# Optimization experiments

Hardware: AMD Instinct MI355X
Metric: run time of the kernel (lower is better)

Reference implementation:

```python
import jax, jax.numpy as jnp
import numpy as np

H = 768
L = 4096
P, KP = 8192, 8
EV, KE = 2048, 6
E = 16384
NR = 32
NUM_LABELS = 2


def setup_inputs() -> dict:
    key = jax.random.key(0)
    ks = jax.random.split(key, 10)
    seq = jax.random.normal(ks[0], (1, L, H), dtype=jnp.float32)
    phrase_idx = jax.random.randint(ks[1], (P, KP), 0, L, dtype=jnp.int32)
    phrase_mask = jnp.ones((P, KP), dtype=jnp.float32)
    event_idx = jax.random.randint(ks[2], (EV, KE), 0, L, dtype=jnp.int32)
    event_mask = jnp.ones((EV, KE), dtype=jnp.float32)
    pair_idx = jax.random.randint(ks[3], (E, 2), 0, EV, dtype=jnp.int32)
    root_idx = jax.random.randint(ks[4], (NR,), 0, P, dtype=jnp.int32)
    s1 = 1.0 / np.sqrt(2 * H)
    W1 = jax.random.normal(ks[5], (2 * H, H), dtype=jnp.float32) * s1
    b1 = jnp.zeros((H,), dtype=jnp.float32)
    Wb = jax.random.normal(ks[6], (2 * H, NUM_LABELS), dtype=jnp.float32) * s1
    bb = jnp.zeros((NUM_LABELS,), dtype=jnp.float32)
    return {"seq": seq, "phrase_idx": phrase_idx, "phrase_mask": phrase_mask,
            "event_idx": event_idx, "event_mask": event_mask, "pair_idx": pair_idx,
            "root_idx": root_idx, "W1": W1, "b1": b1, "Wb": Wb, "bb": bb}


def _masked_mean_gather(tok, idx, mask):
    # tok: [L,H]; idx: [N,K] int; mask: [N,K] float -> [N,H]
    g = tok[idx]                                  # [N,K,H] irregular gather
    s = jnp.einsum('nkh,nk->nh', g, mask)
    d = jnp.maximum(mask.sum(axis=1, keepdims=True), 1.0)
    return s / d


def reference(seq, phrase_idx, phrase_mask, event_idx, event_mask, pair_idx,
              root_idx, W1, b1, Wb, bb):
    tok = seq[0]                                   # [L,H] doc token embeddings
    # phrase embeddings: gather token indices per phrase, masked mean-pool
    ph = _masked_mean_gather(tok, phrase_idx, phrase_mask)   # [P,H]
    # event embeddings: gather span tokens per event, masked mean-pool
    ev = _masked_mean_gather(tok, event_idx, event_mask)     # [EV,H]
    # event-pair nodes: concat the two event embeddings, middle_layer MLP
    e1 = ev[pair_idx[:, 0]]                        # [E,H]
    e2 = ev[pair_idx[:, 1]]                        # [E,H]
    pairs = jnp.concatenate([e1, e2], axis=-1)     # [E,2H]
    node = jax.nn.relu(pairs @ W1 + b1)            # [E,H] (dropout inactive at eval)
    # virtual root: mean of sentence-root phrase embeddings
    vroot = ph[root_idx].mean(axis=0)              # [H]
    feat = jnp.concatenate([node, jnp.broadcast_to(vroot, node.shape)], axis=-1)
    logits = feat @ Wb + bb                        # [E,NUM_LABELS] bilinear classifier
    return logits
```

## Files before the change

### kernel.cpp

```cpp
#include <hip/hip_runtime.h>
#include <hip/hip_bf16.h>

#define H   768
#define H4  192
#define EVN 2048
#define KE  6
#define KP  8
#define EE  16384
#define NR  32

typedef __bf16 v8bf __attribute__((ext_vector_type(8)));
typedef float  v4f  __attribute__((ext_vector_type(4)));

__device__ __forceinline__ void gload16(const void* g, void* lds) {
    __builtin_amdgcn_global_load_lds(
        (const __attribute__((address_space(1))) void*)g,
        (__attribute__((address_space(3))) void*)lds, 16, 0, 0);
}
__device__ __forceinline__ float blo(unsigned u) {
    return __uint_as_float(u << 16);
}
__device__ __forceinline__ float bhi(unsigned u) {
    return __uint_as_float(u & 0xffff0000u);
}

__global__ __launch_bounds__(256) void pre_kernel(
    const float* __restrict__ seq,
    const int* __restrict__ eidx, const float* __restrict__ emask,
    const int* __restrict__ pidx, const float* __restrict__ pmask,
    const int* __restrict__ root_idx, const float* __restrict__ W1,
    __hip_bfloat16* __restrict__ evb, __hip_bfloat16* __restrict__ Wt,
    float* __restrict__ phr) {
    __shared__ float tile[64][65];
    const int b = blockIdx.x;
    const int t = threadIdx.x;
    const float4* seq4 = (const float4*)seq;

    if (b < 512) {
        const int w = t >> 6, l = t & 63;
        const int n = b * 4 + w;
        int idx[KE]; float mk[KE]; float ms = 0.f;
#pragma unroll
        for (int k = 0; k < KE; ++k) {
            idx[k] = eidx[n * KE + k];
            mk[k]  = emask[n * KE + k];
            ms    += mk[k];
        }
        const float inv = 1.f / fmaxf(ms, 1.f);
#pragma unroll
        for (int g = 0; g < 3; ++g) {
            const int t4 = l + g * 64;
            float4 acc = {0.f, 0.f, 0.f, 0.f};
#pragma unroll
            for (int k = 0; k < KE; ++k) {
                float4 v = seq4[idx[k] * H4 + t4];
                acc.x = fmaf(mk[k], v.x, acc.x);
                acc.y = fmaf(mk[k], v.y, acc.y);
                acc.z = fmaf(mk[k], v.z, acc.z);
                acc.w = fmaf(mk[k], v.w, acc.w);
            }
            __hip_bfloat16 o[4];
            o[0] = __float2bfloat16(acc.x * inv);
            o[1] = __float2bfloat16(acc.y * inv);
            o[2] = __float2bfloat16(acc.z * inv);
            o[3] = __float2bfloat16(acc.w * inv);
            *(uint2*)&evb[n * H + t4 * 4] = *(uint2*)o;
        }
    } else if (b < 520) {
        const int w = t >> 6, l = t & 63;
        const int r = (b - 512) * 4 + w;
        const int pr = root_idx[r];
        int idx[KP]; float mk[KP]; float ms = 0.f;
#pragma unroll
        for (int k = 0; k < KP; ++k) {
            idx[k] = pidx[pr * KP + k];
            mk[k]  = pmask[pr * KP + k];
            ms    += mk[k];
        }
        const float inv = 1.f / fmaxf(ms, 1.f);
#pragma unroll
        for (int g = 0; g < 3; ++g) {
            const int t4 = l + g * 64;
            float4 acc = {0.f, 0.f, 0.f, 0.f};
#pragma unroll
            for (int k = 0; k < KP; ++k) {
                float4 v = seq4[idx[k] * H4 + t4];
                acc.x = fmaf(mk[k], v.x, acc.x);
                acc.y = fmaf(mk[k], v.y, acc.y);
                acc.z = fmaf(mk[k], v.z, acc.z);
                acc.w = fmaf(mk[k], v.w, acc.w);
            }
            float4 o = {acc.x * inv, acc.y * inv, acc.z * inv, acc.w * inv};
            ((float4*)phr)[r * H4 + t4] = o;
        }
    } else {
        const int b2 = b - 520;
        const int k0 = (b2 % 12) * 64;
        const int j0 = (b2 / 12) * 64;
        const int s  = (j0 >= H) ? H : 0;
        const int n0 = j0 - s;
        const int c  = t & 63;
        const int r0 = t >> 6;
#pragma unroll
        for (int i = 0; i < 16; ++i) {
            const int r = r0 + i * 4;
            tile[r][c] = W1[(size_t)(s + k0 + r) * H + n0 + c];
        }
        __syncthreads();
#pragma unroll
        for (int i = 0; i < 16; ++i) {
            const int r = r0 + i * 4;
            Wt[(size_t)(j0 + r) * H + k0 + c] = __float2bfloat16(tile[c][r]);
        }
    }
}

__global__ __launch_bounds__(256) void gemm_kernel(
    const __hip_bfloat16* __restrict__ evb_,
    const __hip_bfloat16* __restrict__ Wt_,
    const float* __restrict__ b1v,
    const float* __restrict__ phr, const float* __restrict__ Wb,
    const float* __restrict__ bbv,
    __hip_bfloat16* __restrict__ evw, float* __restrict__ cvec) {
    if (blockIdx.x == 384) {
        __shared__ float r0s[256], r1s[256];
        const int t = threadIdx.x;
        float p0 = 0.f, p1 = 0.f;
#pragma unroll
        for (int w = 0; w < 3; ++w) {
            const int d = t + w * 256;
            float s = 0.f;
            for (int r = 0; r < NR; ++r) s += phr[r * H + d];
            const float v = s * (1.0f / NR);
            p0 = fmaf(v, Wb[(H + d) * 2 + 0], p0);
            p1 = fmaf(v, Wb[(H + d) * 2 + 1], p1);
        }
        r0s[t] = p0; r1s[t] = p1;
        __syncthreads();
        for (int off = 128; off > 0; off >>= 1) {
            if (t < off) { r0s[t] += r0s[t + off]; r1s[t] += r1s[t + off]; }
            __syncthreads();
        }
        if (t == 0) { cvec[0] = r0s[0] + bbv[0]; cvec[1] = r1s[0] + bbv[1]; }
        return;
    }

    __shared__ short As[2][8192];
    __shared__ short Bs[2][4096];
    const short* evb = (const short*)evb_;
    const short* Wt  = (const short*)Wt_;

    const int bid = blockIdx.x;
    const int swz = (bid & 7) * 48 + (bid >> 3);
    const int mt = swz / 24, nt = swz % 24;
    const int m0 = mt * 128, n0 = nt * 64;

    const int t = threadIdx.x;
    const int l = t & 63;
    const int w = t >> 6;
    const int wr = (w >> 1) * 64;
    const int wc = (w & 1) * 32;

    const short* aSrc[4]; int aOff[4];
    const short* bSrc[2]; int bOff[2];
#pragma unroll
    for (int c = 0; c < 4; ++c) {
        const int s = c * 256 + t;
        const int r = s >> 3, pg = s & 7, g = pg ^ (r & 7);
        aSrc[c] = evb + (size_t)(m0 + r) * H + g * 8;
        aOff[c] = s * 16;
    }
#pragma unroll
    for (int c = 0; c < 2; ++c) {
        const int s = c * 256 + t;
        const int r = s >> 3, pg = s & 7, g = pg ^ (r & 7);
        bSrc[c] = Wt + (size_t)(n0 + r) * H + g * 8;
        bOff[c] = s * 16;
    }

    const int fr = l & 15, gq = l >> 4, xm = fr & 7;
    int aRow[4], bRow[2];
#pragma unroll
    for (int mi = 0; mi < 4; ++mi) aRow[mi] = (wr + mi * 16 + fr) * 64;
#pragma unroll
    for (int nj = 0; nj < 2; ++nj) bRow[nj] = (wc + nj * 16 + fr) * 64;
    const int pga = (gq ^ xm) * 8;
    const int pgb = ((4 + gq) ^ xm) * 8;

    v4f acc[4][2] = {};

#pragma unroll
    for (int c = 0; c < 4; ++c) gload16(aSrc[c], (char*)As[0] + aOff[c]);
#pragma unroll
    for (int c = 0; c < 2; ++c) gload16(bSrc[c], (char*)Bs[0] + bOff[c]);
    __syncthreads();

    for (int ks = 0; ks < 12; ++ks) {
        const int cur = ks & 1;
        if (ks < 11) {
#pragma unroll
            for (int c = 0; c < 4; ++c)
                gload16(aSrc[c] + (ks + 1) * 64, (char*)As[cur ^ 1] + aOff[c]);
#pragma unroll
            for (int c = 0; c < 2; ++c)
                gload16(bSrc[c] + (ks + 1) * 64, (char*)Bs[cur ^ 1] + bOff[c]);
        }
        const short* Ab = As[cur];
        const short* Bb = Bs[cur];
        {
            v8bf a0 = *(const v8bf*)(Ab + aRow[0] + pga);
            v8bf a1 = *(const v8bf*)(Ab + aRow[1] + pga);
            v8bf a2 = *(const v8bf*)(Ab + aRow[2] + pga);
            v8bf a3 = *(const v8bf*)(Ab + aRow[3] + pga);
            v8bf b0 = *(const v8bf*)(Bb + bRow[0] + pga);
            v8bf b1 = *(const v8bf*)(Bb + bRow[1] + pga);
            acc[0][0] = __builtin_amdgcn_mfma_f32_16x16x32_bf16(a0, b0, acc[0][0], 0, 0, 0);
            acc[0][1] = __builtin_amdgcn_mfma_f32_16x16x32_bf16(a0, b1, acc[0][1], 0, 0, 0);
            acc[1][0] = __builtin_amdgcn_mfma_f32_16x16x32_bf16(a1, b0, acc[1][0], 0, 0, 0);
            acc[1][1] = __builtin_amdgcn_mfma_f32_16x16x32_bf16(a1, b1, acc[1][1], 0, 0, 0);
            acc[2][0] = __builtin_amdgcn_mfma_f32_16x16x32_bf16(a2, b0, acc[2][0], 0, 0, 0);
            acc[2][1] = __builtin_amdgcn_mfma_f32_16x16x32_bf16(a2, b1, acc[2][1], 0, 0, 0);
            acc[3][0] = __builtin_amdgcn_mfma_f32_16x16x32_bf16(a3, b0, acc[3][0], 0, 0, 0);
            acc[3][1] = __builtin_amdgcn_mfma_f32_16x16x32_bf16(a3, b1, acc[3][1], 0, 0, 0);
        }
        {
            v8bf a0 = *(const v8bf*)(Ab + aRow[0] + pgb);
            v8bf a1 = *(const v8bf*)(Ab + aRow[1] + pgb);
            v8bf a2 = *(const v8bf*)(Ab + aRow[2] + pgb);
            v8bf a3 = *(const v8bf*)(Ab + aRow[3] + pgb);
            v8bf b0 = *(const v8bf*)(Bb + bRow[0] + pgb);
            v8bf b1 = *(const v8bf*)(Bb + bRow[1] + pgb);
            acc[0][0] = __builtin_amdgcn_mfma_f32_16x16x32_bf16(a0, b0, acc[0][0], 0, 0, 0);
            acc[0][1] = __builtin_amdgcn_mfma_f32_16x16x32_bf16(a0, b1, acc[0][1], 0, 0, 0);
            acc[1][0] = __builtin_amdgcn_mfma_f32_16x16x32_bf16(a1, b0, acc[1][0], 0, 0, 0);
            acc[1][1] = __builtin_amdgcn_mfma_f32_16x16x32_bf16(a1, b1, acc[1][1], 0, 0, 0);
            acc[2][0] = __builtin_amdgcn_mfma_f32_16x16x32_bf16(a2, b0, acc[2][0], 0, 0, 0);
            acc[2][1] = __builtin_amdgcn_mfma_f32_16x16x32_bf16(a2, b1, acc[2][1], 0, 0, 0);
            acc[3][0] = __builtin_amdgcn_mfma_f32_16x16x32_bf16(a3, b0, acc[3][0], 0, 0, 0);
            acc[3][1] = __builtin_amdgcn_mfma_f32_16x16x32_bf16(a3, b1, acc[3][1], 0, 0, 0);
        }
        __syncthreads();
    }

    float bv[2];
#pragma unroll
    for (int nj = 0; nj < 2; ++nj) {
        const int ocol = n0 + wc + nj * 16 + fr;
        bv[nj] = (ocol >= H) ? b1v[ocol - H] : 0.f;
    }
#pragma unroll
    for (int mi = 0; mi < 4; ++mi)
#pragma unroll
        for (int nj = 0; nj < 2; ++nj) {
            const int ocol = n0 + wc + nj * 16 + fr;
#pragma unroll
            for (int r = 0; r < 4; ++r) {
                const int orow = m0 + wr + mi * 16 + gq * 4 + r;
                evw[(size_t)orow * 1536 + ocol] =
                    __float2bfloat16(acc[mi][nj][r] + bv[nj]);
            }
        }
}

__global__ __launch_bounds__(256) void pair_logits_kernel(
    const __hip_bfloat16* __restrict__ evw_, const int* __restrict__ pair_idx,
    const float* __restrict__ Wb, const float* __restrict__ cvec,
    float* __restrict__ out) {
    const ushort* evw = (const ushort*)evw_;
    const int wave = threadIdx.x >> 6;
    const int lane = threadIdx.x & 63;
    const int i = blockIdx.x * 4 + wave;
    const int p0 = pair_idx[i * 2 + 0];
    const int p1 = pair_idx[i * 2 + 1];
    const ushort* ra = evw + (size_t)p0 * 1536;
    const ushort* rb = evw + (size_t)p1 * 1536 + H;
    float acc0 = 0.f, acc1 = 0.f;
#pragma unroll
    for (int h = 0; h < 2; ++h) {
        const int j = h * 384 + lane * 6;
        uint3 ua = *(const uint3*)(ra + j);
        uint3 ub = *(const uint3*)(rb + j);
        float4 w0 = *(const float4*)(Wb + j * 2);
        float4 w1 = *(const float4*)(Wb + j * 2 + 4);
        float4 w2 = *(const float4*)(Wb + j * 2 + 8);
        float n0 = fmaxf(blo(ua.x) + blo(ub.x), 0.f);
        float n1 = fmaxf(bhi(ua.x) + bhi(ub.x), 0.f);
        float n2 = fmaxf(blo(ua.y) + blo(ub.y), 0.f);
        float n3 = fmaxf(bhi(ua.y) + bhi(ub.y), 0.f);
        float n4 = fmaxf(blo(ua.z) + blo(ub.z), 0.f);
        float n5 = fmaxf(bhi(ua.z) + bhi(ub.z), 0.f);
        acc0 += n0 * w0.x + n1 * w0.z + n2 * w1.x + n3 * w1.z + n4 * w2.x + n5 * w2.z;
        acc1 += n0 * w0.y + n1 * w0.w + n2 * w1.y + n3 * w1.w + n4 * w2.y + n5 * w2.w;
    }
#pragma unroll
    for (int off = 32; off > 0; off >>= 1) {
        acc0 += __shfl_xor(acc0, off, 64);
        acc1 += __shfl_xor(acc1, off, 64);
    }
    if (lane == 0) {
        out[i * 2 + 0] = acc0 + cvec[0];
        out[i * 2 + 1] = acc1 + cvec[1];
    }
}

extern "C" void kernel_launch(void* const* d_in, const int* in_sizes, int n_in,
                              void* d_out, int out_size, void* d_ws, size_t ws_size,
                              hipStream_t stream) {
    const float* seq         = (const float*)d_in[0];
    const int*   phrase_idx  = (const int*)  d_in[1];
    const float* phrase_mask = (const float*)d_in[2];
    const int*   event_idx   = (const int*)  d_in[3];
    const float* event_mask  = (const float*)d_in[4];
    const int*   pair_idx    = (const int*)  d_in[5];
    const int*   root_idx    = (const int*)  d_in[6];
    const float* W1          = (const float*)d_in[7];
    const float* b1          = (const float*)d_in[8];
    const float* Wb          = (const float*)d_in[9];
    const float* bb          = (const float*)d_in[10];
    float* out = (float*)d_out;

    char* wsb = (char*)d_ws;
    __hip_bfloat16* evb = (__hip_bfloat16*)wsb;
    __hip_bfloat16* Wt  = (__hip_bfloat16*)(wsb + 3145728);
    __hip_bfloat16* evw = (__hip_bfloat16*)(wsb + 5505024);
    float* phr = (float*)(wsb + 11796480);
    float* c   = (float*)(wsb + 11894784);

    pre_kernel<<<808, 256, 0, stream>>>(seq, event_idx, event_mask,
                                        phrase_idx, phrase_mask, root_idx,
                                        W1, evb, Wt, phr);
    gemm_kernel<<<385, 256, 0, stream>>>(evb, Wt, b1, phr, Wb, bb, evw, c);
    pair_logits_kernel<<<EE / 4, 256, 0, stream>>>(evw, pair_idx, Wb, c, out);
}
```

Before: 34.39 us.

## Load B operand directly into registers and double K-step to 128

The GEMM no longer stages the weight (B) tile through LDS. Each lane loads its B fragments straight from global memory into double-buffered registers. The A tile K-step grows from 64 to 128 with a 16-way XOR swizzle, which halves the number of barriers and iterations, and the K loop is fully unrolled. This removes the LDS traffic and the LDS writes for B, but it raises VGPR pressure (16 v8bf B registers) and depends on uncoalesced per-lane global loads being hidden by the prefetch.

```diff
diff --git a/kernel.cpp b/kernel.cpp
--- a/kernel.cpp
+++ b/kernel.cpp
@@ -122,8 +122,11 @@
     const float* __restrict__ phr, const float* __restrict__ Wb,
     const float* __restrict__ bbv,
     __hip_bfloat16* __restrict__ evw, float* __restrict__ cvec) {
+    __shared__ short As[2][16384];
+
     if (blockIdx.x == 384) {
-        __shared__ float r0s[256], r1s[256];
+        float* r0s = (float*)&As[0][0];
+        float* r1s = r0s + 256;
         const int t = threadIdx.x;
         float p0 = 0.f, p1 = 0.f;
 #pragma unroll
@@ -145,8 +148,6 @@
         return;
     }
 
-    __shared__ short As[2][8192];
-    __shared__ short Bs[2][4096];
     const short* evb = (const short*)evb_;
     const short* Wt  = (const short*)Wt_;
 
@@ -161,75 +162,63 @@
     const int wr = (w >> 1) * 64;
     const int wc = (w & 1) * 32;
 
-    const short* aSrc[4]; int aOff[4];
-    const short* bSrc[2]; int bOff[2];
-#pragma unroll
-    for (int c = 0; c < 4; ++c) {
+    const short* aSrc[8]; int aOff[8];
+#pragma unroll
+    for (int c = 0; c < 8; ++c) {
         const int s = c * 256 + t;
-        const int r = s >> 3, pg = s & 7, g = pg ^ (r & 7);
+        const int r = s >> 4, pg = s & 15, g = pg ^ (r & 15);
         aSrc[c] = evb + (size_t)(m0 + r) * H + g * 8;
         aOff[c] = s * 16;
     }
-#pragma unroll
-    for (int c = 0; c < 2; ++c) {
-        const int s = c * 256 + t;
-        const int r = s >> 3, pg = s & 7, g = pg ^ (r & 7);
-        bSrc[c] = Wt + (size_t)(n0 + r) * H + g * 8;
-        bOff[c] = s * 16;
-    }
-
-    const int fr = l & 15, gq = l >> 4, xm = fr & 7;
-    int aRow[4], bRow[2];
-#pragma unroll
-    for (int mi = 0; mi < 4; ++mi) aRow[mi] = (wr + mi * 16 + fr) * 64;
-#pragma unroll
-    for (int nj = 0; nj < 2; ++nj) bRow[nj] = (wc + nj * 16 + fr) * 64;
-    const int pga = (gq ^ xm) * 8;
-    const int pgb = ((4 + gq) ^ xm) * 8;
+
+    const int fr = l & 15, gq = l >> 4, xm = fr & 15;
+    int aRowB[4];
+#pragma unroll
+    for (int mi = 0; mi < 4; ++mi) aRowB[mi] = (wr + mi * 16 + fr) * 256;
+
+    const short* bPtr[2];
+#pragma unroll
+    for (int nj = 0; nj < 2; ++nj)
+        bPtr[nj] = Wt + (size_t)(n0 + wc + nj * 16 + fr) * H + gq * 8;
 
     v4f acc[4][2] = {};
-
-#pragma unroll
-    for (int c = 0; c < 4; ++c) gload16(aSrc[c], (char*)As[0] + aOff[c]);
-#pragma unroll
-    for (int c = 0; c < 2; ++c) gload16(bSrc[c], (char*)Bs[0] + bOff[c]);
+    v8bf bEven[2][4], bOdd[2][4];
+
+#pragma unroll
+    for (int nj = 0; nj < 2; ++nj)
+#pragma unroll
+        for (int h = 0; h < 4; ++h)
+            bEven[nj][h] = *(const v8bf*)(bPtr[nj] + h * 32);
+
+#pragma unroll
+    for (int c = 0; c < 8; ++c) gload16(aSrc[c], (char*)As[0] + aOff[c]);
     __syncthreads();
 
-    for (int ks = 0; ks < 12; ++ks) {
+#pragma unroll
+    for (int ks = 0; ks < 6; ++ks) {
         const int cur = ks & 1;
-        if (ks < 11) {
-#pragma unroll
-            for (int c = 0; c < 4; ++c)
-                gload16(aSrc[c] + (ks + 1) * 64, (char*)As[cur ^ 1] + aOff[c]);
-#pragma unroll
-            for (int c = 0; c < 2; ++c)
-                gload16(bSrc[c] + (ks + 1) * 64, (char*)Bs[cur ^ 1] + bOff[c]);
-        }
-        const short* Ab = As[cur];
-        const short* Bb = Bs[cur];
-        {
-            v8bf a0 = *(const v8bf*)(Ab + aRow[0] + pga);
-            v8bf a1 = *(const v8bf*)(Ab + aRow[1] + pga);
-            v8bf a2 = *(const v8bf*)(Ab + aRow[2] + pga);
-            v8bf a3 = *(const v8bf*)(Ab + aRow[3] + pga);
-            v8bf b0 = *(const v8bf*)(Bb + bRow[0] + pga);
-            v8bf b1 = *(const v8bf*)(Bb + bRow[1] + pga);
-            acc[0][0] = __builtin_amdgcn_mfma_f32_16x16x32_bf16(a0, b0, acc[0][0], 0, 0, 0);
-            acc[0][1] = __builtin_amdgcn_mfma_f32_16x16x32_bf16(a0, b1, acc[0][1], 0, 0, 0);
-            acc[1][0] = __builtin_amdgcn_mfma_f32_16x16x32_bf16(a1, b0, acc[1][0], 0, 0, 0);
-            acc[1][1] = __builtin_amdgcn_mfma_f32_16x16x32_bf16(a1, b1, acc[1][1], 0, 0, 0);
-            acc[2][0] = __builtin_amdgcn_mfma_f32_16x16x32_bf16(a2, b0, acc[2][0], 0, 0, 0);
-            acc[2][1] = __builtin_amdgcn_mfma_f32_16x16x32_bf16(a2, b1, acc[2][1], 0, 0, 0);
-            acc[3][0] = __builtin_amdgcn_mfma_f32_16x16x32_bf16(a3, b0, acc[3][0], 0, 0, 0);
-            acc[3][1] = __builtin_amdgcn_mfma_f32_16x16x32_bf16(a3, b1, acc[3][1], 0, 0, 0);
-        }
-        {
-            v8bf a0 = *(const v8bf*)(Ab + aRow[0] + pgb);
-            v8bf a1 = *(const v8bf*)(Ab + aRow[1] + pgb);
-            v8bf a2 = *(const v8bf*)(Ab + aRow[2] + pgb);
-            v8bf a3 = *(const v8bf*)(Ab + aRow[3] + pgb);
-            v8bf b0 = *(const v8bf*)(Bb + bRow[0] + pgb);
-            v8bf b1 = *(const v8bf*)(Bb + bRow[1] + pgb);
+        if (ks < 5) {
+#pragma unroll
+            for (int c = 0; c < 8; ++c)
+                gload16(aSrc[c] + (ks + 1) * 128, (char*)As[cur ^ 1] + aOff[c]);
+#pragma unroll
+            for (int nj = 0; nj < 2; ++nj)
+#pragma unroll
+                for (int h = 0; h < 4; ++h) {
+                    v8bf v = *(const v8bf*)(bPtr[nj] + (ks + 1) * 128 + h * 32);
+                    if (cur) bEven[nj][h] = v; else bOdd[nj][h] = v;
+                }
+        }
+        const char* Ab = (const char*)As[cur];
+#pragma unroll
+        for (int h = 0; h < 4; ++h) {
+            const int pgo = ((h * 4 + gq) ^ xm) * 16;
+            v8bf a0 = *(const v8bf*)(Ab + aRowB[0] + pgo);
+            v8bf a1 = *(const v8bf*)(Ab + aRowB[1] + pgo);
+            v8bf a2 = *(const v8bf*)(Ab + aRowB[2] + pgo);
+            v8bf a3 = *(const v8bf*)(Ab + aRowB[3] + pgo);
+            v8bf b0 = cur ? bOdd[0][h] : bEven[0][h];
+            v8bf b1 = cur ? bOdd[1][h] : bEven[1][h];
             acc[0][0] = __builtin_amdgcn_mfma_f32_16x16x32_bf16(a0, b0, acc[0][0], 0, 0, 0);
             acc[0][1] = __builtin_amdgcn_mfma_f32_16x16x32_bf16(a0, b1, acc[0][1], 0, 0, 0);
             acc[1][0] = __builtin_amdgcn_mfma_f32_16x16x32_bf16(a1, b0, acc[1][0], 0, 0, 0);
```

Result: slower. 39.16 us (+13.9%).
